# Kernel optimization log

Measured on AMD Instinct MI355X. Metric: run time of the kernel, lower is better.

The kernel has to match this reference:

```python
import jax, jax.numpy as jnp
import numpy as np

EPS_IN = 1e-5   # torch InstanceNorm2d default eps
EPS_VAR = 1e-6  # clamp floor on attention-weighted variance


def _inorm(x):
    # x: (b, c, t); InstanceNorm2d with affine=False normalizes over spatial dims
    m = x.mean(axis=-1, keepdims=True)
    v = x.var(axis=-1, keepdims=True)  # biased variance, matches torch eval-mode IN
    return (x - m) / jnp.sqrt(v + EPS_IN)


def setup_inputs() -> dict:
    key = jax.random.key(0)
    ks = jax.random.split(key, 9)
    b, t, d = 4, 4096, 256
    sc = 1.0 / np.sqrt(d).astype(np.float32)
    return {
        "fc": jax.random.normal(ks[0], (b, t, d), jnp.float32),
        "fs": jax.random.normal(ks[1], (b, t, d), jnp.float32),
        "fcs": jax.random.normal(ks[2], (b, t, d), jnp.float32),
        "Wf": jax.random.normal(ks[3], (d, d), jnp.float32) * sc,
        "bf": jax.random.normal(ks[4], (d,), jnp.float32) * 0.01,
        "Wg": jax.random.normal(ks[5], (d, d), jnp.float32) * sc,
        "bg": jax.random.normal(ks[6], (d,), jnp.float32) * 0.01,
        "Wh": jax.random.normal(ks[7], (d, d), jnp.float32) * sc,
        "bh": jax.random.normal(ks[8], (d,), jnp.float32) * 0.01,
    }


def reference(fc, fs, fcs, Wf, bf, Wg, bg, Wh, bh):
    # (b, t, d) -> channel-first flat (b, d, t); 1x1 conv == per-token linear
    fc_t = jnp.swapaxes(fc, 1, 2)
    fs_t = jnp.swapaxes(fs, 1, 2)
    fcs_t = jnp.swapaxes(fcs, 1, 2)

    Q = jnp.einsum('oc,bct->bto', Wf, _inorm(fc_t)) + bf                 # (b,t,d)
    K = jnp.einsum('oc,bct->bot', Wg, _inorm(fs_t)) + bg[None, :, None]  # (b,d,t)
    V = jnp.einsum('oc,bct->bto', Wh, fs_t) + bh                         # (b,t,d)

    A = jax.nn.softmax(jnp.einsum('btd,bdu->btu', Q, K), axis=-1)        # (b,t,t)
    M = jnp.einsum('btu,bud->btd', A, V)                                 # mean
    Var = jnp.einsum('btu,bud->btd', A, V * V) - M * M                   # E[v^2]-E[v]^2
    S = jnp.sqrt(jnp.maximum(Var, EPS_VAR))

    out_t = jnp.swapaxes(S, 1, 2) * _inorm(fcs_t) + jnp.swapaxes(M, 1, 2)  # (b,d,t)
    return jnp.swapaxes(out_t, 1, 2)  # (b, t, d)
```

## Files before the change

### kernel.cpp

```cpp
#include <hip/hip_runtime.h>
#include <math.h>

#define B 4
#define T 4096
#define D 256
#define NCH 16
#define CHT (T / NCH)
#define KC 32
#define NCHUNK (T / KC)

typedef __attribute__((ext_vector_type(8))) _Float16 half8;
typedef __attribute__((ext_vector_type(4))) _Float16 half4;
typedef __attribute__((ext_vector_type(4))) float f32x4;

__global__ __launch_bounds__(256) void k_prep(
    const float* __restrict__ fc, const float* __restrict__ fs,
    const float* __restrict__ fcs, float* __restrict__ part,
    const float* __restrict__ Wf, const float* __restrict__ Wg,
    const float* __restrict__ Wh, _Float16* __restrict__ Whi,
    _Float16* __restrict__ Wlo)
{
    int blk = blockIdx.x;
    if (blk < 192) {
        int tensor = blk / (B * NCH);
        int rem = blk % (B * NCH);
        int b = rem / NCH, ch = rem % NCH;
        const float* x = (tensor == 0) ? fc : ((tensor == 1) ? fs : fcs);
        int c = threadIdx.x;
        const float* p = x + ((size_t)b * T + (size_t)ch * CHT) * D + c;
        float s = 0.f, ss = 0.f;
        for (int t = 0; t < CHT; ++t) {
            float v = p[(size_t)t * D];
            s += v; ss += v * v;
        }
        float* o = part + (((size_t)tensor * B + b) * NCH + ch) * 2 * D;
        o[c] = s;
        o[D + c] = ss;
    } else {
        int base = (blk - 192) * 2048;
        #pragma unroll
        for (int i = 0; i < 8; ++i) {
            int idx = base + threadIdx.x + i * 256;
            int which = idx >> 16, rc = idx & 65535;
            const float* Wsrc = (which == 0) ? Wf : ((which == 1) ? Wg : Wh);
            float v = Wsrc[rc];
            _Float16 h = (_Float16)v;
            float l = v - (float)h;
            Whi[idx] = h;
            Wlo[idx] = (_Float16)l;
        }
    }
}

__global__ __launch_bounds__(256) void k_stats_final(
    const float* __restrict__ part, float* __restrict__ stats)
{
    int blk = blockIdx.x;
    int tensor = blk / B, b = blk % B;
    int c = threadIdx.x;
    const float* pp = part + (((size_t)tensor * B + b) * NCH) * 2 * D;
    float s = 0.f, ss = 0.f;
    for (int ch = 0; ch < NCH; ++ch) {
        s  += pp[(size_t)ch * 2 * D + c];
        ss += pp[(size_t)ch * 2 * D + D + c];
    }
    float mean = s / (float)T;
    float var  = ss / (float)T - mean * mean;
    float rstd = rsqrtf(var + 1e-5f);
    float* st = stats + (size_t)tensor * 2 * B * D;
    st[(size_t)b * D + c]          = mean;
    st[(size_t)B * D + b * D + c]  = rstd;
}

__global__ __launch_bounds__(256) void k_gemm3(
    const float* __restrict__ fc, const float* __restrict__ fs,
    const _Float16* __restrict__ Whi, const _Float16* __restrict__ Wlo,
    const float* __restrict__ bf, const float* __restrict__ bg,
    const float* __restrict__ bh, const float* __restrict__ stats,
    _Float16* __restrict__ Qg, _Float16* __restrict__ Kg,
    _Float16* __restrict__ oV, _Float16* __restrict__ oV2h,
    _Float16* __restrict__ oV2l)
{
    __shared__ _Float16 Xl[64 * 256];
    const int which = blockIdx.x >> 8;
    const int m0 = (blockIdx.x & 255) * 64;
    const int b = m0 / T;
    const int tid = threadIdx.x;
    const float* x = (which == 0) ? fc : fs;
    const float* bias = (which == 0) ? bf : ((which == 1) ? bg : bh);
    const _Float16* Wh_ = Whi + which * 65536;
    const _Float16* Wl_ = Wlo + which * 65536;
    const int use_norm = (which != 2);
    const float* mean = stats + (which == 0 ? 0 : 1) * 2 * B * D;
    const float* rstd = mean + B * D;

    #pragma unroll
    for (int j = 0; j < 16; ++j) {
        int idx = tid + j * 256;
        int m = idx >> 6, c4 = idx & 63;
        float4 v = *(const float4*)(x + ((size_t)(m0 + m)) * D + c4 * 4);
        if (use_norm) {
            int c = c4 * 4;
            v.x = (v.x - mean[b * D + c + 0]) * rstd[b * D + c + 0];
            v.y = (v.y - mean[b * D + c + 1]) * rstd[b * D + c + 1];
            v.z = (v.z - mean[b * D + c + 2]) * rstd[b * D + c + 2];
            v.w = (v.w - mean[b * D + c + 3]) * rstd[b * D + c + 3];
        }
        half4 h;
        h[0] = (_Float16)v.x; h[1] = (_Float16)v.y;
        h[2] = (_Float16)v.z; h[3] = (_Float16)v.w;
        *(half4*)&Xl[m * 256 + ((c4 * 4) ^ ((m & 7) << 3))] = h;
    }
    __syncthreads();

    const int l = tid & 63, w = tid >> 6;
    const int lo16 = l & 15, hi4 = l >> 4;
    const int row = w * 16 + lo16;

    float bias_v[16];
    #pragma unroll
    for (int nt = 0; nt < 16; ++nt) bias_v[nt] = bias[nt * 16 + lo16];

    f32x4 acc[16];
    #pragma unroll
    for (int nt = 0; nt < 16; ++nt) acc[nt] = (f32x4){0.f, 0.f, 0.f, 0.f};

    #pragma unroll
    for (int kk = 0; kk < 8; ++kk) {
        half8 a = *(const half8*)&Xl[row * 256 + ((kk * 32 + hi4 * 8) ^ ((row & 7) << 3))];
        #pragma unroll
        for (int nt = 0; nt < 16; ++nt) {
            size_t wo = (size_t)(nt * 16 + lo16) * 256 + kk * 32 + hi4 * 8;
            half8 bhf = *(const half8*)(Wh_ + wo);
            acc[nt] = __builtin_amdgcn_mfma_f32_16x16x32_f16(a, bhf, acc[nt], 0, 0, 0);
            half8 blf = *(const half8*)(Wl_ + wo);
            acc[nt] = __builtin_amdgcn_mfma_f32_16x16x32_f16(a, blf, acc[nt], 0, 0, 0);
        }
    }

    if (which != 2) {
        _Float16* out1 = (which == 0) ? Qg : Kg;
        #pragma unroll
        for (int nt = 0; nt < 16; ++nt)
            #pragma unroll
            for (int r = 0; r < 4; ++r) {
                int t = m0 + w * 16 + hi4 * 4 + r;
                out1[(size_t)t * D + nt * 16 + lo16] = (_Float16)(acc[nt][r] + bias_v[nt]);
            }
    } else {
        int t0 = (m0 % T) + w * 16 + hi4 * 4;
        #pragma unroll
        for (int nt = 0; nt < 16; ++nt) {
            int o = nt * 16 + lo16;
            half4 vh, h4, l4;
            #pragma unroll
            for (int r = 0; r < 4; ++r) {
                float v = acc[nt][r] + bias_v[nt];
                _Float16 vhh = (_Float16)v;
                float f2 = (float)vhh * (float)vhh;
                _Float16 hh = (_Float16)f2;
                float fl = f2 - (float)hh;
                vh[r] = vhh; h4[r] = hh; l4[r] = (_Float16)fl;
            }
            size_t base = ((size_t)b * D + o) * T + t0;
            *(half4*)(oV   + base) = vh;
            *(half4*)(oV2h + base) = h4;
            *(half4*)(oV2l + base) = l4;
        }
    }
}

__global__ __launch_bounds__(512, 1) void k_attn(
    const _Float16* __restrict__ Qg, const _Float16* __restrict__ Kg,
    const _Float16* __restrict__ Vtg, const _Float16* __restrict__ V2hg,
    const _Float16* __restrict__ V2lg, const float* __restrict__ fcs,
    const float* __restrict__ stats_fcs, float* __restrict__ out)
{
    __shared__ __align__(16) _Float16 Kl [2][32 * 256];
    __shared__ __align__(16) _Float16 Vl [2][256 * 32];
    __shared__ __align__(16) _Float16 V2h[2][256 * 32];
    __shared__ __align__(16) _Float16 V2l[2][256 * 32];
    __shared__ __align__(16) _Float16 Pl [2][64 * 32];
    __shared__ float corr_lds[2][64];
    __shared__ float l_lds[64];
    __shared__ int   flags[2][4];

    const int tid = threadIdx.x;
    const int l = tid & 63;
    const int w = tid >> 6;
    const int swz = (blockIdx.x & 7) * 32 + (blockIdx.x >> 3);
    const int b  = swz >> 6;
    const int q0 = (swz & 63) << 6;
    const int lo16 = l & 15, hi4 = l >> 4;

    const _Float16* KgB  = Kg   + (size_t)b * T * D;
    const _Float16* VtB  = Vtg  + (size_t)b * D * T;
    const _Float16* V2hB = V2hg + (size_t)b * D * T;
    const _Float16* V2lB = V2lg + (size_t)b * D * T;

    half8 qf[8];
    if (w < 4) {
        const _Float16* qp = Qg + ((size_t)(b * T + q0 + 16 * w + lo16)) * D + hi4 * 8;
        #pragma unroll
        for (int kk = 0; kk < 8; ++kk) qf[kk] = *(const half8*)(qp + kk * 32);
    }

    f32x4 accM[4][2], accE[4][2];
    #pragma unroll
    for (int qs = 0; qs < 4; ++qs)
        #pragma unroll
        for (int jj = 0; jj < 2; ++jj) {
            accM[qs][jj] = (f32x4){0.f, 0.f, 0.f, 0.f};
            accE[qs][jj] = (f32x4){0.f, 0.f, 0.f, 0.f};
        }
    float m_run[4] = {-1e9f, -1e9f, -1e9f, -1e9f};
    float lv[4] = {0.f, 0.f, 0.f, 0.f};

    const int t2 = tid & 255;
    half8 vr[4], vhr[4], vlr[4];

    auto do_pv = [&](int pb) {
        #pragma unroll
        for (int qs = 0; qs < 4; ++qs) {
            if (flags[pb][qs]) {
                #pragma unroll
                for (int r = 0; r < 4; ++r) {
                    float c = corr_lds[pb][qs * 16 + hi4 * 4 + r];
                    accM[qs][0][r] *= c; accM[qs][1][r] *= c;
                    accE[qs][0][r] *= c; accE[qs][1][r] *= c;
                }
            }
        }
        half8 pa[4];
        #pragma unroll
        for (int qs = 0; qs < 4; ++qs) {
            int q = qs * 16 + lo16;
            pa[qs] = *(const half8*)&Pl[pb][q * 32 + ((hi4 ^ (q & 3)) << 3)];
        }
        __builtin_amdgcn_s_setprio(1);
        #pragma unroll
        for (int jj = 0; jj < 2; ++jj) {
            int d = (2 * w + jj) * 16 + lo16;
            int p = d * 32 + ((hi4 ^ ((d >> 1) & 3)) << 3);
            half8 bh  = *(const half8*)&Vl[pb][p];
            half8 b2h = *(const half8*)&V2h[pb][p];
            half8 b2l = *(const half8*)&V2l[pb][p];
            #pragma unroll
            for (int qs = 0; qs < 4; ++qs) {
                accM[qs][jj] = __builtin_amdgcn_mfma_f32_16x16x32_f16(pa[qs], bh,  accM[qs][jj], 0, 0, 0);
                accE[qs][jj] = __builtin_amdgcn_mfma_f32_16x16x32_f16(pa[qs], b2h, accE[qs][jj], 0, 0, 0);
                accE[qs][jj] = __builtin_amdgcn_mfma_f32_16x16x32_f16(pa[qs], b2l, accE[qs][jj], 0, 0, 0);
            }
        }
        __builtin_amdgcn_s_setprio(0);
    };

    if (w >= 4) {
        half8 kr0[4];
        #pragma unroll
        for (int i = 0; i < 4; ++i) {
            int g = t2 + i * 256;
            kr0[i] = *(const half8*)(KgB + (size_t)(g >> 5) * D + (g & 31) * 8);
        }
        #pragma unroll
        for (int i = 0; i < 4; ++i) {
            int g = t2 + i * 256; int d = g >> 2, kg = g & 3;
            size_t off = (size_t)d * T + kg * 8;
            vr[i]  = *(const half8*)(VtB  + off);
            vhr[i] = *(const half8*)(V2hB + off);
            vlr[i] = *(const half8*)(V2lB + off);
        }
        #pragma unroll
        for (int i = 0; i < 4; ++i) {
            int g = t2 + i * 256; int rr = g >> 5, cg = g & 31;
            *(half8*)&Kl[0][rr * 256 + ((cg ^ (rr & 7)) << 3)] = kr0[i];
        }
    }
    __syncthreads();

    for (int kc = 0; kc < NCHUNK; ++kc) {
        const int cb = kc & 1, pb = cb ^ 1;

        if (w < 4) {
            f32x4 c0 = (f32x4){0.f, 0.f, 0.f, 0.f}, c1 = (f32x4){0.f, 0.f, 0.f, 0.f};
            __builtin_amdgcn_s_setprio(1);
            #pragma unroll
            for (int kk = 0; kk < 8; ++kk) {
                int cg = kk * 4 + hi4;
                half8 b0 = *(const half8*)&Kl[cb][lo16 * 256 + ((cg ^ (lo16 & 7)) << 3)];
                half8 b1 = *(const half8*)&Kl[cb][(16 + lo16) * 256 + ((cg ^ ((16 + lo16) & 7)) << 3)];
                c0 = __builtin_amdgcn_mfma_f32_16x16x32_f16(qf[kk], b0, c0, 0, 0, 0);
                c1 = __builtin_amdgcn_mfma_f32_16x16x32_f16(qf[kk], b1, c1, 0, 0, 0);
            }
            __builtin_amdgcn_s_setprio(0);

            if (kc > 0) do_pv(pb);

            float cm[4];
            #pragma unroll
            for (int r = 0; r < 4; ++r) cm[r] = fmaxf(c0[r], c1[r]);
            float tmax = fmaxf(fmaxf(cm[0] - m_run[0], cm[1] - m_run[1]),
                               fmaxf(cm[2] - m_run[2], cm[3] - m_run[3]));
            int flagv = 0;
            if (__any(tmax > 10.f)) {
                flagv = 1;
                float corr[4];
                #pragma unroll
                for (int r = 0; r < 4; ++r) {
                    float rm = cm[r];
                    rm = fmaxf(rm, __shfl_xor(rm, 1));
                    rm = fmaxf(rm, __shfl_xor(rm, 2));
                    rm = fmaxf(rm, __shfl_xor(rm, 4));
                    rm = fmaxf(rm, __shfl_xor(rm, 8));
                    float mn = fmaxf(m_run[r], rm);
                    corr[r] = __expf(m_run[r] - mn);
                    m_run[r] = mn;
                    lv[r] *= corr[r];
                }
                if (lo16 == 0) {
                    #pragma unroll
                    for (int r = 0; r < 4; ++r)
                        corr_lds[cb][w * 16 + hi4 * 4 + r] = corr[r];
                }
            }
            if (l == 0) flags[cb][w] = flagv;

            float p0[4], p1[4];
            #pragma unroll
            for (int r = 0; r < 4; ++r) {
                p0[r] = __expf(c0[r] - m_run[r]);
                p1[r] = __expf(c1[r] - m_run[r]);
                lv[r] += p0[r] + p1[r];
            }
            #pragma unroll
            for (int r = 0; r < 4; ++r) {
                int q = 16 * w + hi4 * 4 + r;
                int ka = lo16, kb = 16 + lo16;
                Pl[cb][q * 32 + (((ka >> 3) ^ (q & 3)) << 3) + (ka & 7)] = (_Float16)p0[r];
                Pl[cb][q * 32 + (((kb >> 3) ^ (q & 3)) << 3) + (kb & 7)] = (_Float16)p1[r];
            }
        } else {
            #pragma unroll
            for (int i = 0; i < 4; ++i) {
                int g = t2 + i * 256; int d = g >> 2, kg = g & 3;
                int p = d * 32 + ((kg ^ ((d >> 1) & 3)) << 3);
                *(half8*)&Vl[cb][p]  = vr[i];
                *(half8*)&V2h[cb][p] = vhr[i];
                *(half8*)&V2l[cb][p] = vlr[i];
            }

            half8 kr[4];
            const bool doK = (kc + 1 < NCHUNK);
            if (doK) {
                int kn = (kc + 1) * KC;
                #pragma unroll
                for (int i = 0; i < 4; ++i) {
                    int g = t2 + i * 256;
                    kr[i] = *(const half8*)(KgB + (size_t)(kn + (g >> 5)) * D + (g & 31) * 8);
                }
                #pragma unroll
                for (int i = 0; i < 4; ++i) {
                    int g = t2 + i * 256; int d = g >> 2, kg = g & 3;
                    size_t off = (size_t)d * T + kn + kg * 8;
                    vr[i]  = *(const half8*)(VtB  + off);
                    vhr[i] = *(const half8*)(V2hB + off);
                    vlr[i] = *(const half8*)(V2lB + off);
                }
            }

            if (kc > 0) do_pv(pb);

            if (doK) {
                #pragma unroll
                for (int i = 0; i < 4; ++i) {
                    int g = t2 + i * 256; int rr = g >> 5, cg = g & 31;
                    *(half8*)&Kl[cb ^ 1][rr * 256 + ((cg ^ (rr & 7)) << 3)] = kr[i];
                }
            }
        }
        __syncthreads();
    }

    do_pv((NCHUNK - 1) & 1);

    if (w < 4) {
        #pragma unroll
        for (int r = 0; r < 4; ++r) {
            float lr = lv[r];
            lr += __shfl_xor(lr, 1);
            lr += __shfl_xor(lr, 2);
            lr += __shfl_xor(lr, 4);
            lr += __shfl_xor(lr, 8);
            if (lo16 == 0) l_lds[w * 16 + hi4 * 4 + r] = lr;
        }
    }
    __syncthreads();

    const float* mfc = stats_fcs;
    const float* rfc = stats_fcs + B * D;
    #pragma unroll
    for (int qs = 0; qs < 4; ++qs) {
        #pragma unroll
        for (int r = 0; r < 4; ++r) {
            float linv = 1.f / l_lds[qs * 16 + hi4 * 4 + r];
            int q = q0 + qs * 16 + hi4 * 4 + r;
            size_t rowb = ((size_t)(b * T + q)) * D;
            #pragma unroll
            for (int jj = 0; jj < 2; ++jj) {
                int d = (2 * w + jj) * 16 + lo16;
                float M  = accM[qs][jj][r] * linv;
                float E2 = accE[qs][jj][r] * linv;
                float S  = sqrtf(fmaxf(E2 - M * M, 1e-6f));
                float f  = fcs[rowb + d];
                out[rowb + d] = S * ((f - mfc[b * D + d]) * rfc[b * D + d]) + M;
            }
        }
    }
}

extern "C" void kernel_launch(void* const* d_in, const int* in_sizes, int n_in,
                              void* d_out, int out_size, void* d_ws, size_t ws_size,
                              hipStream_t stream)
{
    const float* fc  = (const float*)d_in[0];
    const float* fs  = (const float*)d_in[1];
    const float* fcs = (const float*)d_in[2];
    const float* Wf  = (const float*)d_in[3];
    const float* bf  = (const float*)d_in[4];
    const float* Wg  = (const float*)d_in[5];
    const float* bg  = (const float*)d_in[6];
    const float* Wh  = (const float*)d_in[7];
    const float* bh  = (const float*)d_in[8];
    float* out = (float*)d_out;

    char* ws = (char*)d_ws;
    float* stats = (float*)ws;
    float* part  = (float*)(ws + (64 << 10));
    _Float16* Whi = (_Float16*)(ws + (512 << 10));
    _Float16* Wlo = Whi + 3 * 65536;
    _Float16* Qg   = (_Float16*)(ws + (2 << 20));
    _Float16* Kg   = Qg  + (size_t)B * T * D;
    _Float16* Vtg  = Kg  + (size_t)B * T * D;
    _Float16* V2hg = Vtg + (size_t)B * T * D;
    _Float16* V2lg = V2hg + (size_t)B * T * D;

    k_prep<<<288, 256, 0, stream>>>(fc, fs, fcs, part, Wf, Wg, Wh, Whi, Wlo);
    k_stats_final<<<3 * B, 256, 0, stream>>>(part, stats);

    float* st_fcs = stats + 2 * 2 * B * D;

    k_gemm3<<<3 * 256, 256, 0, stream>>>(fc, fs, Whi, Wlo, bf, bg, bh, stats,
                                         Qg, Kg, Vtg, V2hg, V2lg);

    k_attn<<<B * (T / 64), 512, 0, stream>>>(Qg, Kg, Vtg, V2hg, V2lg, fcs, st_fcs, out);
}
```

Before: 321.0 us.

## Rebalance PV MFMA work: QK waves take one d-tile, loader waves three

Splits the 16 output d-tiles unevenly between wave groups. The four QK/softmax waves now own one d-tile each, while the four loader waves own three each, replacing the even split of two per wave. The QK waves' PV step is also moved ahead of their QK^T MFMAs under raised priority. The aim is to take MFMA work off the softmax-critical waves and hand it to the loader waves, which were idle. In exchange the loader waves hold more accumulator registers (24 f32x4), which may cost occupancy, and the correction scaling relies on flags from the previous chunk.

```diff
diff --git a/kernel.cpp b/kernel.cpp
--- a/kernel.cpp
+++ b/kernel.cpp
@@ -205,11 +205,11 @@
         for (int kk = 0; kk < 8; ++kk) qf[kk] = *(const half8*)(qp + kk * 32);
     }
 
-    f32x4 accM[4][2], accE[4][2];
+    f32x4 accM[4][3], accE[4][3];
     #pragma unroll
     for (int qs = 0; qs < 4; ++qs)
         #pragma unroll
-        for (int jj = 0; jj < 2; ++jj) {
+        for (int jj = 0; jj < 3; ++jj) {
             accM[qs][jj] = (f32x4){0.f, 0.f, 0.f, 0.f};
             accE[qs][jj] = (f32x4){0.f, 0.f, 0.f, 0.f};
         }
@@ -217,17 +217,17 @@
     float lv[4] = {0.f, 0.f, 0.f, 0.f};
 
     const int t2 = tid & 255;
+    const int tb = 4 + (w - 4) * 3;
     half8 vr[4], vhr[4], vlr[4];
 
-    auto do_pv = [&](int pb) {
+    auto do_pv_A = [&](int pb) {
         #pragma unroll
         for (int qs = 0; qs < 4; ++qs) {
             if (flags[pb][qs]) {
                 #pragma unroll
                 for (int r = 0; r < 4; ++r) {
                     float c = corr_lds[pb][qs * 16 + hi4 * 4 + r];
-                    accM[qs][0][r] *= c; accM[qs][1][r] *= c;
-                    accE[qs][0][r] *= c; accE[qs][1][r] *= c;
+                    accM[qs][0][r] *= c; accE[qs][0][r] *= c;
                 }
             }
         }
@@ -237,10 +237,40 @@
             int q = qs * 16 + lo16;
             pa[qs] = *(const half8*)&Pl[pb][q * 32 + ((hi4 ^ (q & 3)) << 3)];
         }
+        int d = w * 16 + lo16;
+        int p = d * 32 + ((hi4 ^ ((d >> 1) & 3)) << 3);
+        half8 bh  = *(const half8*)&Vl[pb][p];
+        half8 b2h = *(const half8*)&V2h[pb][p];
+        half8 b2l = *(const half8*)&V2l[pb][p];
+        #pragma unroll
+        for (int qs = 0; qs < 4; ++qs) {
+            accM[qs][0] = __builtin_amdgcn_mfma_f32_16x16x32_f16(pa[qs], bh,  accM[qs][0], 0, 0, 0);
+            accE[qs][0] = __builtin_amdgcn_mfma_f32_16x16x32_f16(pa[qs], b2h, accE[qs][0], 0, 0, 0);
+            accE[qs][0] = __builtin_amdgcn_mfma_f32_16x16x32_f16(pa[qs], b2l, accE[qs][0], 0, 0, 0);
+        }
+    };
+    auto do_pv_B = [&](int pb) {
+        #pragma unroll
+        for (int qs = 0; qs < 4; ++qs) {
+            if (flags[pb][qs]) {
+                #pragma unroll
+                for (int r = 0; r < 4; ++r) {
+                    float c = corr_lds[pb][qs * 16 + hi4 * 4 + r];
+                    #pragma unroll
+                    for (int jj = 0; jj < 3; ++jj) { accM[qs][jj][r] *= c; accE[qs][jj][r] *= c; }
+                }
+            }
+        }
+        half8 pa[4];
+        #pragma unroll
+        for (int qs = 0; qs < 4; ++qs) {
+            int q = qs * 16 + lo16;
+            pa[qs] = *(const half8*)&Pl[pb][q * 32 + ((hi4 ^ (q & 3)) << 3)];
+        }
         __builtin_amdgcn_s_setprio(1);
         #pragma unroll
-        for (int jj = 0; jj < 2; ++jj) {
-            int d = (2 * w + jj) * 16 + lo16;
+        for (int jj = 0; jj < 3; ++jj) {
+            int d = (tb + jj) * 16 + lo16;
             int p = d * 32 + ((hi4 ^ ((d >> 1) & 3)) << 3);
             half8 bh  = *(const half8*)&Vl[pb][p];
             half8 b2h = *(const half8*)&V2h[pb][p];
@@ -284,6 +314,7 @@
         if (w < 4) {
             f32x4 c0 = (f32x4){0.f, 0.f, 0.f, 0.f}, c1 = (f32x4){0.f, 0.f, 0.f, 0.f};
             __builtin_amdgcn_s_setprio(1);
+            if (kc > 0) do_pv_A(pb);
             #pragma unroll
             for (int kk = 0; kk < 8; ++kk) {
                 int cg = kk * 4 + hi4;
@@ -293,8 +324,6 @@
                 c1 = __builtin_amdgcn_mfma_f32_16x16x32_f16(qf[kk], b1, c1, 0, 0, 0);
             }
             __builtin_amdgcn_s_setprio(0);
-
-            if (kc > 0) do_pv(pb);
 
             float cm[4];
             #pragma unroll
@@ -368,7 +397,7 @@
                 }
             }
 
-            if (kc > 0) do_pv(pb);
+            if (kc > 0) do_pv_B(pb);
 
             if (doK) {
                 #pragma unroll
@@ -381,7 +410,8 @@
         __syncthreads();
     }
 
-    do_pv((NCHUNK - 1) & 1);
+    if (w < 4) do_pv_A((NCHUNK - 1) & 1);
+    else       do_pv_B((NCHUNK - 1) & 1);
 
     if (w < 4) {
         #pragma unroll
@@ -398,21 +428,39 @@
 
     const float* mfc = stats_fcs;
     const float* rfc = stats_fcs + B * D;
-    #pragma unroll
-    for (int qs = 0; qs < 4; ++qs) {
-        #pragma unroll
-        for (int r = 0; r < 4; ++r) {
-            float linv = 1.f / l_lds[qs * 16 + hi4 * 4 + r];
-            int q = q0 + qs * 16 + hi4 * 4 + r;
-            size_t rowb = ((size_t)(b * T + q)) * D;
-            #pragma unroll
-            for (int jj = 0; jj < 2; ++jj) {
-                int d = (2 * w + jj) * 16 + lo16;
-                float M  = accM[qs][jj][r] * linv;
-                float E2 = accE[qs][jj][r] * linv;
+    if (w < 4) {
+        int d = w * 16 + lo16;
+        #pragma unroll
+        for (int qs = 0; qs < 4; ++qs) {
+            #pragma unroll
+            for (int r = 0; r < 4; ++r) {
+                float linv = 1.f / l_lds[qs * 16 + hi4 * 4 + r];
+                int q = q0 + qs * 16 + hi4 * 4 + r;
+                size_t rowb = ((size_t)(b * T + q)) * D;
+                float M  = accM[qs][0][r] * linv;
+                float E2 = accE[qs][0][r] * linv;
                 float S  = sqrtf(fmaxf(E2 - M * M, 1e-6f));
                 float f  = fcs[rowb + d];
                 out[rowb + d] = S * ((f - mfc[b * D + d]) * rfc[b * D + d]) + M;
+            }
+        }
+    } else {
+        #pragma unroll
+        for (int qs = 0; qs < 4; ++qs) {
+            #pragma unroll
+            for (int r = 0; r < 4; ++r) {
+                float linv = 1.f / l_lds[qs * 16 + hi4 * 4 + r];
+                int q = q0 + qs * 16 + hi4 * 4 + r;
+                size_t rowb = ((size_t)(b * T + q)) * D;
+                #pragma unroll
+                for (int jj = 0; jj < 3; ++jj) {
+                    int d = (tb + jj) * 16 + lo16;
+                    float M  = accM[qs][jj][r] * linv;
+                    float E2 = accE[qs][jj][r] * linv;
+                    float S  = sqrtf(fmaxf(E2 - M * M, 1e-6f));
+                    float f  = fcs[rowb + d];
+                    out[rowb + d] = S * ((f - mfc[b * D + d]) * rfc[b * D + d]) + M;
+                }
             }
         }
     }
```

Result: slower. 438.2 us (+36.5%).
